# Optimization experiments

Hardware: AMD Instinct MI355X
Metric: run time of the kernel (lower is better)

Reference implementation:

```python
import jax, jax.numpy as jnp
import numpy as np

B, CIN, H, W = 16, 16, 320, 320
OUT, KS, K = 16, 3, 4
HIDDEN = int(CIN * 0.25) + 1  # 5, matches attention2d
PAD = 1


def setup_inputs() -> dict:
    key = jax.random.key(0)
    k1, k2, k3, k4 = jax.random.split(key, 4)
    x = jax.random.normal(k1, (B, CIN, H, W), dtype=jnp.float32)
    # attention2d params: fc1 (1x1 conv, no bias), fc2 (1x1 conv, bias)
    w1 = jax.random.normal(k2, (HIDDEN, CIN), dtype=jnp.float32) * (2.0 / CIN) ** 0.5
    w2 = jax.random.normal(k3, (K * OUT, HIDDEN), dtype=jnp.float32) * (2.0 / HIDDEN) ** 0.5
    b2 = jnp.zeros((K * OUT,), dtype=jnp.float32)
    # expert weight bank [out, in//groups, ks, ks, K]
    weight = jax.random.normal(k4, (OUT, CIN, KS, KS, K), dtype=jnp.float32) * (1.0 / (CIN * KS * KS)) ** 0.5
    return {"x": x, "w1": w1, "w2": w2, "b2": b2, "weight": weight}


def reference(x, w1, w2, b2, weight):
    b, cin, h, w = x.shape
    out_p, cin_g, ks, _, kk = weight.shape
    # attention2d: global avg pool -> 1x1 conv -> relu -> 1x1 conv (+bias)
    pooled = x.mean(axis=(2, 3))                       # [B, Cin]
    hid = jax.nn.relu(pooled @ w1.T)                   # [B, hidden]
    attn = hid @ w2.T + b2                             # [B, K*out]
    # softmax over K experts per output channel
    s = jax.nn.softmax(attn.reshape(b, kk, out_p), axis=1)  # [B, K, out]
    # faithful to the torch conv2d grouping trick: flat layout is (k, o),
    # then group o consumes flat channels [o*K:(o+1)*K]
    coeffs = s.reshape(b, -1).reshape(b, out_p, kk)    # [B, out, K]
    # per-sample mixed kernels
    wmix = jnp.einsum('bok,ocxyk->bocxy', coeffs, weight)  # [B, out, in//g, ks, ks]
    # per-sample grouped conv via feature_group_count = B * groups (groups=1)
    xg = x.reshape(1, b * cin, h, w)
    wg = wmix.reshape(b * out_p, cin_g, ks, ks)
    out = jax.lax.conv_general_dilated(
        xg, wg, window_strides=(1, 1), padding=((PAD, PAD), (PAD, PAD)),
        feature_group_count=b, dimension_numbers=('NCHW', 'OIHW', 'NCHW'))
    return out.reshape(b, out_p, out.shape[-2], out.shape[-1])
```

## Files before the change

kernel.cpp:

```cpp
#include <hip/hip_runtime.h>
#include <hip/hip_bf16.h>
#include <math.h>

#define BB   16
#define CIN  16
#define HH   320
#define WW   320
#define OUTC 16
#define KK   4
#define HID  5
#define HWSZ (HH * WW)

#define TW   64
#define TH   16
#define LROW 66
#define LROWS 18
#define NPIX (LROWS * LROW)
#define NTASK (2 * NPIX)
#define LDSN (2 * NPIX * 8)
#define KCH  5

typedef __attribute__((ext_vector_type(8))) short bf16x8_t;
typedef __attribute__((ext_vector_type(4))) float f32x4_t;

static __device__ __forceinline__ unsigned short f2bf(float f) {
    union { float f; unsigned u; } x; x.f = f;
    unsigned r = x.u + 0x7FFF + ((x.u >> 16) & 1);
    return (unsigned short)(r >> 16);
}

__global__ __launch_bounds__(1024)
void dg_pool_kernel(const float* __restrict__ x, float* __restrict__ pooled) {
    const int plane = blockIdx.x;
    const float4* p4 = (const float4*)(x + (size_t)plane * HWSZ);
    float s = 0.f;
    #pragma unroll 5
    for (int i = threadIdx.x; i < HWSZ / 4; i += 1024) {
        float4 v = p4[i];
        s += (v.x + v.y) + (v.z + v.w);
    }
    #pragma unroll
    for (int off = 32; off > 0; off >>= 1) s += __shfl_down(s, off, 64);
    __shared__ float red[16];
    if ((threadIdx.x & 63) == 0) red[threadIdx.x >> 6] = s;
    __syncthreads();
    if (threadIdx.x == 0) {
        float t = 0.f;
        #pragma unroll
        for (int i = 0; i < 16; ++i) t += red[i];
        pooled[plane] = t * (1.f / (float)HWSZ);
    }
}

__global__ __launch_bounds__(64)
void dg_mix_kernel(const float* __restrict__ pooled,
                   const float* __restrict__ w1,
                   const float* __restrict__ w2,
                   const float* __restrict__ b2,
                   const float* __restrict__ weight,
                   unsigned short* __restrict__ wB) {
    const int b = blockIdx.x;
    const int tid = threadIdx.x;
    __shared__ float sm[64];
    __shared__ float coeff[64];

    float pb[CIN];
    #pragma unroll
    for (int c = 0; c < CIN; ++c) pb[c] = pooled[b * CIN + c];
    float hid[HID];
    #pragma unroll
    for (int h = 0; h < HID; ++h) {
        float a = 0.f;
        #pragma unroll
        for (int c = 0; c < CIN; ++c) a = fmaf(pb[c], w1[h * CIN + c], a);
        hid[h] = fmaxf(a, 0.f);
    }
    float a = b2[tid];
    #pragma unroll
    for (int h = 0; h < HID; ++h) a = fmaf(hid[h], w2[tid * HID + h], a);
    sm[tid] = a;
    __syncthreads();

    const int oa = tid & 15;
    float a0 = sm[oa], a1 = sm[16 + oa], a2 = sm[32 + oa], a3 = sm[48 + oa];
    float m = fmaxf(fmaxf(a0, a1), fmaxf(a2, a3));
    float denom = expf(a0 - m) + expf(a1 - m) + expf(a2 - m) + expf(a3 - m);
    coeff[tid] = expf(sm[tid] - m) / denom;
    __syncthreads();

    const int o = tid & 15;
    const int kbase = (tid >> 4) * 8;
    #pragma unroll
    for (int kc = 0; kc < KCH; ++kc) {
        unsigned short frag[8];
        #pragma unroll
        for (int j = 0; j < 8; ++j) {
            const int k = kc * 32 + kbase + j;
            float v = 0.f;
            if (k < 144) {
                const int tap = k >> 4;
                const int c = k & 15;
                const float* wp = weight + (((size_t)(o * CIN + c) * 9 + tap) << 2);
                v = coeff[o * 4 + 0] * wp[0] + coeff[o * 4 + 1] * wp[1]
                  + coeff[o * 4 + 2] * wp[2] + coeff[o * 4 + 3] * wp[3];
            }
            frag[j] = f2bf(v);
        }
        unsigned short* dst = wB + (((size_t)(b * KCH + kc) * 64) + tid) * 8;
        #pragma unroll
        for (int j = 0; j < 8; ++j) dst[j] = frag[j];
    }
}

__global__ __launch_bounds__(256, 4)
void dg_conv_kernel(const float* __restrict__ x,
                    const unsigned short* __restrict__ wB,
                    float* __restrict__ out) {
    const int b   = blockIdx.z;
    const int by0 = blockIdx.y * TH;
    const int bx0 = blockIdx.x * TW;
    const int tid = threadIdx.x;
    const int lane = tid & 63;
    const int wave = tid >> 6;

    __shared__ __align__(16) unsigned short sx[LDSN];

    bf16x8_t Bf[KCH];
    {
        const unsigned short* wBb = wB + (size_t)b * KCH * 512;
        #pragma unroll
        for (int kc = 0; kc < KCH; ++kc)
            Bf[kc] = *(const bf16x8_t*)(wBb + kc * 512 + lane * 8);
    }

    {
        const float* xb = x + (size_t)b * CIN * HWSZ;
        #pragma unroll 1
        for (int it = 0; it < 10; ++it) {
            const int t = tid + it * 256;
            if (t < NTASK) {
                const int half = (t >= NPIX) ? 1 : 0;
                const int P    = t - half * NPIX;
                const int row  = P / LROW;
                const int px   = P - row * LROW;
                const int gy = by0 - 1 + row;
                const int gx = bx0 - 1 + px;
                const bool valid = ((unsigned)gy < HH) && ((unsigned)gx < WW);
                const int gyc = valid ? gy : 0;
                const int gxc = valid ? gx : 0;
                const float* bp = xb + (size_t)(half * 8) * HWSZ
                                     + (size_t)gyc * WW + gxc;
                bf16x8_t v8;
                #pragma unroll
                for (int j = 0; j < 8; ++j) {
                    float v = valid ? bp[(size_t)j * HWSZ] : 0.f;
                    v8[j] = (short)f2bf(v);
                }
                *(bf16x8_t*)&sx[(size_t)t * 8] = v8;
            }
        }
    }

    const int m     = lane & 15;
    const int quad  = lane >> 4;
    const int chalf = quad & 1;
    int dP[KCH];
    #pragma unroll
    for (int kc = 0; kc < KCH; ++kc) {
        int t = 2 * kc + (quad >> 1);
        if (t > 8) t = 8;
        dP[kc] = (t / 3 - 1) * LROW + (t % 3 - 1);
    }
    const int hofs = chalf * NPIX;

    f32x4_t acc[16];
    #pragma unroll
    for (int i = 0; i < 16; ++i) acc[i] = (f32x4_t){0.f, 0.f, 0.f, 0.f};

    __syncthreads();

    #pragma unroll
    for (int rr = 0; rr < 4; ++rr) {
        #pragma unroll
        for (int tx = 0; tx < 4; ++tx) {
            const int P0 = (4 * wave + rr + 1) * LROW + 1 + tx * 16 + m;
            #pragma unroll
            for (int kc = 0; kc < KCH; ++kc) {
                const int S = hofs + P0 + dP[kc];
                const bf16x8_t Af = *(const bf16x8_t*)&sx[(size_t)S * 8];
                acc[rr * 4 + tx] = __builtin_amdgcn_mfma_f32_16x16x32_bf16(
                    Af, Bf[kc], acc[rr * 4 + tx], 0, 0, 0);
            }
        }
    }

    const int n = lane & 15;
    float* ob = out + ((size_t)(b * OUTC + n)) * HWSZ;
    #pragma unroll
    for (int rr = 0; rr < 4; ++rr) {
        const int gy = by0 + 4 * wave + rr;
        #pragma unroll
        for (int tx = 0; tx < 4; ++tx) {
            const int gx = bx0 + tx * 16 + quad * 4;
            *(f32x4_t*)(ob + (size_t)gy * WW + gx) = acc[rr * 4 + tx];
        }
    }
}

extern "C" void kernel_launch(void* const* d_in, const int* in_sizes, int n_in,
                              void* d_out, int out_size, void* d_ws, size_t ws_size,
                              hipStream_t stream) {
    const float* x      = (const float*)d_in[0];
    const float* w1     = (const float*)d_in[1];
    const float* w2     = (const float*)d_in[2];
    const float* b2     = (const float*)d_in[3];
    const float* weight = (const float*)d_in[4];
    float* out = (float*)d_out;

    float* pooled = (float*)d_ws;
    unsigned short* wBf = (unsigned short*)((float*)d_ws + 256);

    dg_pool_kernel<<<BB * CIN, 1024, 0, stream>>>(x, pooled);
    dg_mix_kernel<<<BB, 64, 0, stream>>>(pooled, w1, w2, b2, weight, wBf);
    dg_conv_kernel<<<dim3(WW / TW, HH / TH, BB), 256, 0, stream>>>(x, wBf, out);
}
```

Baseline: 239.9 us.

## Fuse pooling with bf16 channel-interleaved transpose and stage conv tiles via global_load_lds

A new prep kernel reads x once and does two jobs: it computes per-block partial channel sums for pooling, and it writes x as bf16 in a channel-interleaved layout, 8 channels per 16-byte pixel. The mix kernel reduces the partials, and the conv kernel fills LDS with direct 16-byte global_load_lds copies from that layout. Out-of-bounds pixels point at a zero page instead of doing eight strided fp32 loads and a conversion per pixel. The cost is an extra ~52MB workspace write and read, traded for cheaper and more coalesced tile staging. It falls back to the old path when the workspace is too small.

Result: faster. 228.7 us (-4.7%).

```diff
diff --git a/kernel.cpp b/kernel.cpp
--- a/kernel.cpp
+++ b/kernel.cpp
@@ -20,6 +20,15 @@
 #define LDSN (2 * NPIX * 8)
 #define KCH  5
 
+#define K1_BLOCKS_PER_B 100
+#define K1_GROUPS_PER_BLOCK 512
+
+#define XT_BYTES      52428800ull
+#define PART_OFF      52428800ull
+#define ZPAGE_OFF     52480000ull
+#define WB_OFF        52480064ull
+#define WS_NEED       (WB_OFF + 81920ull)
+
 typedef __attribute__((ext_vector_type(8))) short bf16x8_t;
 typedef __attribute__((ext_vector_type(4))) float f32x4_t;
 
@@ -27,6 +36,228 @@
     union { float f; unsigned u; } x; x.f = f;
     unsigned r = x.u + 0x7FFF + ((x.u >> 16) & 1);
     return (unsigned short)(r >> 16);
+}
+
+__global__ __launch_bounds__(256)
+void dg_prep_kernel(const float* __restrict__ x,
+                    unsigned short* __restrict__ xT,
+                    float* __restrict__ partials) {
+    const int blk = blockIdx.x;
+    const int b   = blk / K1_BLOCKS_PER_B;
+    const int bib = blk - b * K1_BLOCKS_PER_B;
+    const int half = (bib >= 50) ? 1 : 0;
+    const int gbase = (bib - half * 50) * K1_GROUPS_PER_BLOCK;
+    const int tid = threadIdx.x;
+
+    const float* xb = x + ((size_t)(b * CIN + half * 8)) * HWSZ;
+    unsigned short* xTb = xT + (((size_t)(b * 2 + half)) * HWSZ) * 8;
+
+    float sums[8];
+    #pragma unroll
+    for (int c = 0; c < 8; ++c) sums[c] = 0.f;
+
+    #pragma unroll 1
+    for (int it = 0; it < 2; ++it) {
+        const int g = gbase + it * 256 + tid;
+        const int p0 = g * 4;
+        f32x4_t v[8];
+        #pragma unroll
+        for (int c = 0; c < 8; ++c) {
+            v[c] = *(const f32x4_t*)(xb + (size_t)c * HWSZ + p0);
+            sums[c] += (v[c][0] + v[c][1]) + (v[c][2] + v[c][3]);
+        }
+        #pragma unroll
+        for (int j = 0; j < 4; ++j) {
+            bf16x8_t o;
+            #pragma unroll
+            for (int c = 0; c < 8; ++c) o[c] = (short)f2bf(v[c][j]);
+            *(bf16x8_t*)(xTb + ((size_t)(p0 + j) << 3)) = o;
+        }
+    }
+
+    #pragma unroll
+    for (int c = 0; c < 8; ++c) {
+        float s = sums[c];
+        #pragma unroll
+        for (int off = 32; off > 0; off >>= 1) s += __shfl_down(s, off, 64);
+        sums[c] = s;
+    }
+    __shared__ float red[4][8];
+    if ((tid & 63) == 0) {
+        #pragma unroll
+        for (int c = 0; c < 8; ++c) red[tid >> 6][c] = sums[c];
+    }
+    __syncthreads();
+    if (tid < 8) {
+        float t = red[0][tid] + red[1][tid] + red[2][tid] + red[3][tid];
+        partials[(size_t)blk * 8 + tid] = t;
+    }
+}
+
+__global__ __launch_bounds__(64)
+void dg_mix2_kernel(const float* __restrict__ partials,
+                    const float* __restrict__ w1,
+                    const float* __restrict__ w2,
+                    const float* __restrict__ b2,
+                    const float* __restrict__ weight,
+                    unsigned short* __restrict__ wB,
+                    float* __restrict__ zpage) {
+    const int b = blockIdx.x;
+    const int tid = threadIdx.x;
+    __shared__ float pooledSh[16];
+    __shared__ float sm[64];
+    __shared__ float coeff[64];
+
+    if (tid < 16) {
+        const int half = tid >> 3;
+        const float* pp = partials
+            + ((size_t)(b * K1_BLOCKS_PER_B + half * 50)) * 8 + (tid & 7);
+        float s = 0.f;
+        #pragma unroll
+        for (int i = 0; i < 50; ++i) s += pp[(size_t)i * 8];
+        pooledSh[tid] = s * (1.f / (float)HWSZ);
+    }
+    if (b == 0 && tid < 16) zpage[tid] = 0.f;
+    __syncthreads();
+
+    float pb[CIN];
+    #pragma unroll
+    for (int c = 0; c < CIN; ++c) pb[c] = pooledSh[c];
+    float hid[HID];
+    #pragma unroll
+    for (int h = 0; h < HID; ++h) {
+        float a = 0.f;
+        #pragma unroll
+        for (int c = 0; c < CIN; ++c) a = fmaf(pb[c], w1[h * CIN + c], a);
+        hid[h] = fmaxf(a, 0.f);
+    }
+    float a = b2[tid];
+    #pragma unroll
+    for (int h = 0; h < HID; ++h) a = fmaf(hid[h], w2[tid * HID + h], a);
+    sm[tid] = a;
+    __syncthreads();
+
+    const int oa = tid & 15;
+    float a0 = sm[oa], a1 = sm[16 + oa], a2 = sm[32 + oa], a3 = sm[48 + oa];
+    float m = fmaxf(fmaxf(a0, a1), fmaxf(a2, a3));
+    float denom = expf(a0 - m) + expf(a1 - m) + expf(a2 - m) + expf(a3 - m);
+    coeff[tid] = expf(sm[tid] - m) / denom;
+    __syncthreads();
+
+    const int o = tid & 15;
+    const int kbase = (tid >> 4) * 8;
+    #pragma unroll
+    for (int kc = 0; kc < KCH; ++kc) {
+        unsigned short frag[8];
+        #pragma unroll
+        for (int j = 0; j < 8; ++j) {
+            const int k = kc * 32 + kbase + j;
+            float v = 0.f;
+            if (k < 144) {
+                const int tap = k >> 4;
+                const int c = k & 15;
+                const float* wp = weight + (((size_t)(o * CIN + c) * 9 + tap) << 2);
+                v = coeff[o * 4 + 0] * wp[0] + coeff[o * 4 + 1] * wp[1]
+                  + coeff[o * 4 + 2] * wp[2] + coeff[o * 4 + 3] * wp[3];
+            }
+            frag[j] = f2bf(v);
+        }
+        unsigned short* dst = wB + (((size_t)(b * KCH + kc) * 64) + tid) * 8;
+        #pragma unroll
+        for (int j = 0; j < 8; ++j) dst[j] = frag[j];
+    }
+}
+
+__global__ __launch_bounds__(256, 4)
+void dg_conv_bf16_kernel(const unsigned short* __restrict__ xT,
+                         const unsigned short* __restrict__ wB,
+                         const unsigned short* __restrict__ zpage,
+                         float* __restrict__ out) {
+    const int b   = blockIdx.z;
+    const int by0 = blockIdx.y * TH;
+    const int bx0 = blockIdx.x * TW;
+    const int tid = threadIdx.x;
+    const int lane = tid & 63;
+    const int wave = tid >> 6;
+
+    __shared__ __align__(16) unsigned short sx[LDSN];
+
+    bf16x8_t Bf[KCH];
+    {
+        const unsigned short* wBb = wB + (size_t)b * KCH * 512;
+        #pragma unroll
+        for (int kc = 0; kc < KCH; ++kc)
+            Bf[kc] = *(const bf16x8_t*)(wBb + kc * 512 + lane * 8);
+    }
+
+    {
+        const unsigned short* xTb = xT + (size_t)b * 2 * HWSZ * 8;
+        #pragma unroll 1
+        for (int it = 0; it < 10; ++it) {
+            int t = tid + it * 256;
+            if (t >= NTASK) t -= 256;
+            const int half = (t >= NPIX) ? 1 : 0;
+            const int P    = t - half * NPIX;
+            const int row  = P / LROW;
+            const int px   = P - row * LROW;
+            const int gy = by0 - 1 + row;
+            const int gx = bx0 - 1 + px;
+            const bool valid = ((unsigned)gy < HH) && ((unsigned)gx < WW);
+            const int lin = gy * WW + gx;
+            const unsigned short* src = valid
+                ? xTb + (((size_t)half * HWSZ + (size_t)lin) << 3)
+                : zpage;
+            __builtin_amdgcn_global_load_lds(
+                (const __attribute__((address_space(1))) void*)src,
+                (__attribute__((address_space(3))) void*)&sx[(size_t)t * 8],
+                16, 0, 0);
+        }
+    }
+
+    const int m     = lane & 15;
+    const int quad  = lane >> 4;
+    const int chalf = quad & 1;
+    int dP[KCH];
+    #pragma unroll
+    for (int kc = 0; kc < KCH; ++kc) {
+        int t = 2 * kc + (quad >> 1);
+        if (t > 8) t = 8;
+        dP[kc] = (t / 3 - 1) * LROW + (t % 3 - 1);
+    }
+    const int hofs = chalf * NPIX;
+
+    f32x4_t acc[16];
+    #pragma unroll
+    for (int i = 0; i < 16; ++i) acc[i] = (f32x4_t){0.f, 0.f, 0.f, 0.f};
+
+    __syncthreads();
+
+    #pragma unroll
+    for (int rr = 0; rr < 4; ++rr) {
+        #pragma unroll
+        for (int tx = 0; tx < 4; ++tx) {
+            const int P0 = (4 * wave + rr + 1) * LROW + 1 + tx * 16 + m;
+            #pragma unroll
+            for (int kc = 0; kc < KCH; ++kc) {
+                const int S = hofs + P0 + dP[kc];
+                const bf16x8_t Af = *(const bf16x8_t*)&sx[(size_t)S * 8];
+                acc[rr * 4 + tx] = __builtin_amdgcn_mfma_f32_16x16x32_bf16(
+                    Af, Bf[kc], acc[rr * 4 + tx], 0, 0, 0);
+            }
+        }
+    }
+
+    const int n = lane & 15;
+    float* ob = out + ((size_t)(b * OUTC + n)) * HWSZ;
+    #pragma unroll
+    for (int rr = 0; rr < 4; ++rr) {
+        const int gy = by0 + 4 * wave + rr;
+        #pragma unroll
+        for (int tx = 0; tx < 4; ++tx) {
+            const int gx = bx0 + tx * 16 + quad * 4;
+            *(f32x4_t*)(ob + (size_t)gy * WW + gx) = acc[rr * 4 + tx];
+        }
+    }
 }
 
 __global__ __launch_bounds__(1024)
@@ -217,10 +448,22 @@
     const float* weight = (const float*)d_in[4];
     float* out = (float*)d_out;
 
-    float* pooled = (float*)d_ws;
-    unsigned short* wBf = (unsigned short*)((float*)d_ws + 256);
-
-    dg_pool_kernel<<<BB * CIN, 1024, 0, stream>>>(x, pooled);
-    dg_mix_kernel<<<BB, 64, 0, stream>>>(pooled, w1, w2, b2, weight, wBf);
-    dg_conv_kernel<<<dim3(WW / TW, HH / TH, BB), 256, 0, stream>>>(x, wBf, out);
-}
+    if (ws_size >= WS_NEED) {
+        unsigned short* xT       = (unsigned short*)d_ws;
+        float*          partials = (float*)((char*)d_ws + PART_OFF);
+        float*          zpage    = (float*)((char*)d_ws + ZPAGE_OFF);
+        unsigned short* wBf      = (unsigned short*)((char*)d_ws + WB_OFF);
+
+        dg_prep_kernel<<<BB * K1_BLOCKS_PER_B, 256, 0, stream>>>(x, xT, partials);
+        dg_mix2_kernel<<<BB, 64, 0, stream>>>(partials, w1, w2, b2, weight, wBf, zpage);
+        dg_conv_bf16_kernel<<<dim3(WW / TW, HH / TH, BB), 256, 0, stream>>>(
+            xT, wBf, (const unsigned short*)zpage, out);
+    } else {
+        float* pooled = (float*)d_ws;
+        unsigned short* wBf = (unsigned short*)((float*)d_ws + 256);
+
+        dg_pool_kernel<<<BB * CIN, 1024, 0, stream>>>(x, pooled);
+        dg_mix_kernel<<<BB, 64, 0, stream>>>(pooled, w1, w2, b2, weight, wBf);
+        dg_conv_kernel<<<dim3(WW / TW, HH / TH, BB), 256, 0, stream>>>(x, wBf, out);
+    }
+}
```
